# Kernel tuning notes

Hardware: AMD Instinct MI355X
Metric: run time of the kernel (lower is better)

Reference implementation:

```python
import jax, jax.numpy as jnp
import numpy as np

SCORE_THRESH = 0.05
NMS_THRESH = 0.5
K = 1000            # max NMS candidates (fixed for jit; padded/masked)
IMG_W, IMG_H = 1333, 800


def setup_inputs() -> dict:
    key = jax.random.key(0)
    k1, k2, k3 = jax.random.split(key, 3)
    N, C = 200000, 81
    class_logits = jax.random.normal(k1, (N, C), dtype=jnp.float32) * 2.0
    # well-formed xyxy boxes inside the image
    cxcy = jax.random.uniform(k2, (N, 2), dtype=jnp.float32) * jnp.array([IMG_W, IMG_H], jnp.float32)
    wh = jax.random.uniform(k3, (N, 2), dtype=jnp.float32) * 200.0 + 1.0
    boxes = jnp.concatenate([cxcy - wh * 0.5, cxcy + wh * 0.5], axis=-1)
    return {"class_logits": class_logits, "boxes": boxes}


def _pairwise_iou(b):
    # b: [K, 4] xyxy -> [K, K]
    area = (b[:, 2] - b[:, 0]) * (b[:, 3] - b[:, 1])
    lt = jnp.maximum(b[:, None, :2], b[None, :, :2])
    rb = jnp.minimum(b[:, None, 2:], b[None, :, 2:])
    wh = jnp.clip(rb - lt, 0.0)
    inter = wh[..., 0] * wh[..., 1]
    return inter / (area[:, None] + area[None, :] - inter + 1e-9)


def reference(class_logits, boxes):
    N, C = class_logits.shape
    prob = jax.nn.softmax(class_logits, axis=-1)            # [N, C]
    # clip_to_image (TO_REMOVE=1 convention: clamp to size-1)
    bx = jnp.stack([
        jnp.clip(boxes[:, 0], 0.0, IMG_W - 1),
        jnp.clip(boxes[:, 1], 0.0, IMG_H - 1),
        jnp.clip(boxes[:, 2], 0.0, IMG_W - 1),
        jnp.clip(boxes[:, 3], 0.0, IMG_H - 1),
    ], axis=-1)                                             # [N, 4]
    flat = prob.reshape(-1)                                 # [N*C], class = idx % C
    idx = jnp.arange(N * C)
    valid = (flat > SCORE_THRESH) & (idx % C != 0)          # fg + score threshold
    masked = jnp.where(valid, flat, -jnp.inf)
    top_scores, top_idx = jax.lax.top_k(masked, K)          # sorted descending
    prop_idx = top_idx // C
    cls = top_idx % C
    bk = bx[prop_idx]                                       # [K, 4]
    valid_k = jnp.isfinite(top_scores)
    scores_k = jnp.where(valid_k, top_scores, 0.0)
    # class-aware greedy NMS over the (sorted) top-K candidates
    conflict = (_pairwise_iou(bk) > NMS_THRESH) & (cls[:, None] == cls[None, :])
    rng = jnp.arange(K)

    def body(i, keep):
        sup = jnp.any(keep & conflict[:, i] & (rng < i))
        return keep.at[i].set(keep[i] & ~sup)

    keep = jax.lax.fori_loop(0, K, body, valid_k)
    out = jnp.concatenate([bk, scores_k[:, None]], axis=-1) * keep[:, None].astype(bk.dtype)
    return out  # [K, 5]: (x1, y1, x2, y2, score), zeroed where suppressed/invalid
```

## Files before the change

### kernel.cpp

```cpp
#include <hip/hip_runtime.h>
#include <stdint.h>
#include <math.h>

#define N_CLS    81
#define TOPK     1000
#define LISTCAP  (1u << 21)
#define CAP2     16384
#define SCORE_TH 0.05f
#define IMG_W    1333.0f
#define IMG_H    800.0f
#define GH_REP   8

#define GH_BASE  1905

#define OFF_CNT    0
#define OFF_CNT2   8
#define OFF_GH     64
#define OFF_RH     4608
#define OFF_SORTED 8704
#define MEMSET_BYTES 16704
#define OFF_SEL    16768
#define OFF_SEL2   16793984
#define OFF_BOX    16925056
#define OFF_SCORE  16941056
#define OFF_CLS    16945056
#define OFF_MASK   16949056

typedef unsigned long long u64;

__global__ __launch_bounds__(256) void k_pass1(
        const float* __restrict__ logits, int nrows,
        u64* __restrict__ sel, unsigned* __restrict__ cnt,
        unsigned* __restrict__ ghist) {
    __shared__ unsigned lh[128];
    __shared__ u64 cbuf[2048];
    __shared__ unsigned lcnt, gbase;
    int tid = threadIdx.x, wv = tid >> 6, ln = tid & 63;
    for (int i = tid; i < 128; i += 256) lh[i] = 0;
    if (tid == 0) lcnt = 0;
    __syncthreads();

    int stride = gridDim.x * 16;
    for (int base = blockIdx.x * 16 + wv * 4; base < nrows; base += stride) {
        int nr = nrows - base; if (nr > 4) nr = 4;
        float v0[4], v1[4], m[4], e0[4], e1[4], s[4];
        #pragma unroll
        for (int k = 0; k < 4; k++) {
            bool ok = (k < nr);
            const float* rp = logits + (size_t)(ok ? base + k : base) * N_CLS;
            v0[k] = ok ? rp[ln] : 0.0f;
            v1[k] = (ok && ln < N_CLS - 64) ? rp[64 + ln] : -INFINITY;
        }
        #pragma unroll
        for (int k = 0; k < 4; k++) m[k] = fmaxf(v0[k], v1[k]);
        #pragma unroll
        for (int off = 32; off > 0; off >>= 1)
            #pragma unroll
            for (int k = 0; k < 4; k++) m[k] = fmaxf(m[k], __shfl_xor(m[k], off));
        #pragma unroll
        for (int k = 0; k < 4; k++) {
            e0[k] = expf(v0[k] - m[k]);
            e1[k] = (ln < N_CLS - 64) ? expf(v1[k] - m[k]) : 0.0f;
            s[k] = e0[k] + e1[k];
        }
        #pragma unroll
        for (int off = 32; off > 0; off >>= 1)
            #pragma unroll
            for (int k = 0; k < 4; k++) s[k] += __shfl_xor(s[k], off);

        #pragma unroll
        for (int k = 0; k < 4; k++) {
            if (k >= nr) break;
            float p0 = e0[k] / s[k];
            float p1 = e1[k] / s[k];
            bool c0 = (k < nr) && (ln != 0) && (p0 > SCORE_TH);
            bool c1 = (k < nr) && (ln < N_CLS - 64) && (p1 > SCORE_TH);
            unsigned fb0 = __float_as_uint(p0), fb1 = __float_as_uint(p1);
            if (c0) atomicAdd(&lh[(fb0 >> 19) - GH_BASE], 1u);
            if (c1) atomicAdd(&lh[(fb1 >> 19) - GH_BASE], 1u);
            u64 b0 = __ballot(c0), b1 = __ballot(c1);
            int n0 = __popcll(b0), n1 = __popcll(b1);
            if (n0 + n1 == 0) continue;
            unsigned wb = 0;
            if (ln == 0) wb = atomicAdd(&lcnt, (unsigned)(n0 + n1));
            wb = __shfl(wb, 0);
            u64 lt = (1ull << ln) - 1ull;
            unsigned flat = (unsigned)(base + k) * N_CLS + (unsigned)ln;
            if (c0) {
                unsigned pos = wb + (unsigned)__popcll(b0 & lt);
                u64 key = ((u64)fb0 << 32) | (u64)(0xFFFFFFu - flat);
                if (pos < 2048) cbuf[pos] = key;
                else { unsigned gp = atomicAdd(cnt, 1u); if (gp < LISTCAP) sel[gp] = key; }
            }
            if (c1) {
                unsigned pos = wb + (unsigned)n0 + (unsigned)__popcll(b1 & lt);
                u64 key = ((u64)fb1 << 32) | (u64)(0xFFFFFFu - (flat + 64u));
                if (pos < 2048) cbuf[pos] = key;
                else { unsigned gp = atomicAdd(cnt, 1u); if (gp < LISTCAP) sel[gp] = key; }
            }
        }
    }
    __syncthreads();
    unsigned* gh = ghist + (blockIdx.x & (GH_REP - 1)) * 128;
    for (int i = tid; i < 128; i += 256) {
        unsigned v = lh[i];
        if (v) atomicAdd(&gh[i], v);
    }
    unsigned total = lcnt; if (total > 2048u) total = 2048u;
    if (tid == 0) gbase = atomicAdd(cnt, total);
    __syncthreads();
    unsigned gb = gbase;
    for (unsigned i = tid; i < total; i += 256) {
        unsigned gp = gb + i;
        if (gp < LISTCAP) sel[gp] = cbuf[i];
    }
}

__device__ inline int scan_coarse(const unsigned* __restrict__ ghist, unsigned* c_above) {
    unsigned cum = 0;
    for (int i = 127; i >= 0; --i) {
        unsigned c = 0;
        #pragma unroll
        for (int r = 0; r < GH_REP; r++) c += ghist[r * 128 + i];
        if (cum + c >= TOPK) { *c_above = cum; return i; }
        cum += c;
    }
    *c_above = cum;
    return -1;
}

__global__ __launch_bounds__(256) void k_refine(
        const u64* __restrict__ sel, const unsigned* __restrict__ cnt,
        const unsigned* __restrict__ ghist, unsigned* __restrict__ rhist) {
    __shared__ unsigned lh[1024];
    __shared__ int sB;
    int tid = threadIdx.x;
    for (int i = tid; i < 1024; i += 256) lh[i] = 0;
    if (tid == 0) { unsigned ca; sB = scan_coarse(ghist, &ca); }
    __syncthreads();
    int B = sB;
    if (B < 0) return;
    unsigned Bbits = (unsigned)(B + GH_BASE);
    unsigned M = *cnt; if (M > LISTCAP) M = LISTCAP;
    unsigned stride = gridDim.x * blockDim.x;
    for (unsigned i = blockIdx.x * blockDim.x + tid; i < M; i += stride) {
        unsigned bits = (unsigned)(sel[i] >> 32);
        if ((bits >> 19) == Bbits) atomicAdd(&lh[(bits >> 9) & 1023u], 1u);
    }
    __syncthreads();
    for (int i = tid; i < 1024; i += 256) {
        unsigned v = lh[i];
        if (v) atomicAdd(&rhist[i], v);
    }
}

__global__ __launch_bounds__(256) void k_select(
        const u64* __restrict__ sel, const unsigned* __restrict__ cnt,
        const unsigned* __restrict__ ghist, const unsigned* __restrict__ rhist,
        u64* __restrict__ sel2, unsigned* __restrict__ cnt2) {
    __shared__ unsigned s4[256];
    __shared__ unsigned tbs;
    int tid = threadIdx.x, ln = tid & 63;
    unsigned ps = 0;
    #pragma unroll
    for (int k = 0; k < 4; k++) ps += rhist[tid * 4 + k];
    s4[tid] = ps;
    __syncthreads();
    if (tid == 0) {
        unsigned c_above;
        int B = scan_coarse(ghist, &c_above);
        unsigned tb = 0;
        if (B >= 0) {
            unsigned cab = c_above;
            int g = -1;
            for (int i = 255; i >= 0; --i) {
                if (cab + s4[i] >= TOPK) { g = i; break; }
                cab += s4[i];
            }
            int sb = 0;
            if (g >= 0) {
                for (int i = g * 4 + 3; i >= g * 4; --i) {
                    unsigned c = rhist[i];
                    if (cab + c >= TOPK) { sb = i; break; }
                    cab += c;
                }
            }
            tb = ((unsigned)(B + GH_BASE) << 19) | ((unsigned)sb << 9);
        }
        tbs = tb;
    }
    __syncthreads();
    unsigned tb = tbs;
    unsigned M = *cnt; if (M > LISTCAP) M = LISTCAP;
    unsigned stride = gridDim.x * blockDim.x;
    for (unsigned ibase = blockIdx.x * blockDim.x; ibase < M; ibase += stride) {
        unsigned i = ibase + tid;
        bool act = (i < M);
        u64 key = act ? sel[i] : 0ull;
        bool c = act && ((unsigned)(key >> 32) >= tb);
        u64 b = __ballot(c);
        int n = __popcll(b);
        if (n == 0) continue;
        unsigned wb = 0;
        if (ln == 0) wb = atomicAdd(cnt2, (unsigned)n);
        wb = __shfl(wb, 0);
        if (c) {
            unsigned pos = wb + (unsigned)__popcll(b & ((1ull << ln) - 1ull));
            if (pos < CAP2) sel2[pos] = key;
        }
    }
}

__global__ __launch_bounds__(256) void k_rank(
        const u64* __restrict__ sel2, const unsigned* __restrict__ cnt2,
        u64* __restrict__ sorted) {
    __shared__ u64 ch[2048];
    unsigned S = *cnt2; if (S > CAP2) S = CAP2;
    if (blockIdx.x * 256u >= S) return;
    unsigned t = blockIdx.x * 256u + threadIdx.x;
    u64 my = (t < S) ? sel2[t] : 0ull;
    int r = 0;
    for (unsigned c0 = 0; c0 < S; c0 += 2048) {
        unsigned n = S - c0; if (n > 2048) n = 2048;
        __syncthreads();
        for (unsigned i = threadIdx.x; i < n; i += 256) ch[i] = sel2[c0 + i];
        __syncthreads();
        if (t < S)
            for (unsigned j = 0; j < n; j++) r += (ch[j] > my) ? 1 : 0;
    }
    if (t < S && r < TOPK) sorted[r] = my;
}

__global__ __launch_bounds__(256) void k_decode(
        const u64* __restrict__ sorted, const float* __restrict__ boxes,
        float* __restrict__ boxK, float* __restrict__ scoreK, int* __restrict__ clsK) {
    int t = blockIdx.x * blockDim.x + threadIdx.x;
    if (t >= TOPK) return;
    u64 key = sorted[t];
    if (key != 0ull) {
        float sc = __uint_as_float((unsigned)(key >> 32));
        unsigned fi = 0xFFFFFFu - (unsigned)(key & 0xFFFFFFFFull);
        unsigned prop = fi / N_CLS;
        int cls = (int)(fi - prop * N_CLS);
        const float* b = boxes + (size_t)prop * 4;
        boxK[t * 4 + 0] = fminf(fmaxf(b[0], 0.0f), IMG_W - 1.0f);
        boxK[t * 4 + 1] = fminf(fmaxf(b[1], 0.0f), IMG_H - 1.0f);
        boxK[t * 4 + 2] = fminf(fmaxf(b[2], 0.0f), IMG_W - 1.0f);
        boxK[t * 4 + 3] = fminf(fmaxf(b[3], 0.0f), IMG_H - 1.0f);
        scoreK[t] = sc;
        clsK[t] = cls;
    } else {
        boxK[t * 4 + 0] = 0.0f; boxK[t * 4 + 1] = 0.0f;
        boxK[t * 4 + 2] = 0.0f; boxK[t * 4 + 3] = 0.0f;
        scoreK[t] = 0.0f;
        clsK[t] = -1;
    }
}

__global__ __launch_bounds__(256) void k_conflict(
        const float* __restrict__ boxK, const int* __restrict__ clsK,
        u64* __restrict__ mask) {
    int t = blockIdx.x * blockDim.x + threadIdx.x;
    if (t >= TOPK * 16) return;
    int i = t >> 4, w = t & 15;
    float x1 = boxK[i * 4 + 0], y1 = boxK[i * 4 + 1];
    float x2 = boxK[i * 4 + 2], y2 = boxK[i * 4 + 3];
    int ci = clsK[i];
    float ai = (x2 - x1) * (y2 - y1);
    u64 m = 0;
    int jbase = w << 6;
    for (int jj = 0; jj < 64; jj++) {
        int j = jbase + jj;
        if (j >= TOPK) break;
        float u1 = boxK[j * 4 + 0], w1 = boxK[j * 4 + 1];
        float u2 = boxK[j * 4 + 2], w2 = boxK[j * 4 + 3];
        float aj = (u2 - u1) * (w2 - w1);
        float ww = fmaxf(fminf(x2, u2) - fmaxf(x1, u1), 0.0f);
        float hh = fmaxf(fminf(y2, w2) - fmaxf(y1, w1), 0.0f);
        float inter = ww * hh;
        float iou = inter / (ai + aj - inter + 1e-9f);
        if (iou > 0.5f && ci == clsK[j]) m |= (1ull << jj);
    }
    mask[(size_t)i * 16 + w] = m;
}

__global__ __launch_bounds__(1024) void k_nms_out(
        const u64* __restrict__ mask, const float* __restrict__ boxK,
        const float* __restrict__ scoreK, float* __restrict__ out) {
    __shared__ u64 words[16];
    __shared__ int changed;
    int tid = threadIdx.x, wv = tid >> 6, ln = tid & 63;
    bool valid = (tid < TOPK) && (scoreK[tid] > 0.0f);
    u64 row[16];
    #pragma unroll
    for (int w = 0; w < 16; w++)
        row[w] = (tid < TOPK) ? mask[(size_t)tid * 16 + w] : 0ull;
    u64 lowmask = (1ull << ln) - 1ull;
    bool keep = valid;
    for (int it = 0; it < 1024; ++it) {
        u64 b = __ballot(keep);
        if (ln == 0) words[wv] = b;
        if (tid == 0) changed = 0;
        __syncthreads();
        u64 sup = 0;
        for (int w = 0; w <= wv; w++) {
            u64 kw = words[w];
            if (w == wv) kw &= lowmask;
            sup |= row[w] & kw;
        }
        bool nk = valid && (sup == 0ull);
        if (nk != keep) changed = 1;
        keep = nk;
        __syncthreads();
        if (!changed) break;
    }
    if (tid < TOPK) {
        float x1 = boxK[tid * 4 + 0], y1 = boxK[tid * 4 + 1];
        float x2 = boxK[tid * 4 + 2], y2 = boxK[tid * 4 + 3];
        float sc = scoreK[tid];
        out[tid * 5 + 0] = keep ? x1 : 0.0f;
        out[tid * 5 + 1] = keep ? y1 : 0.0f;
        out[tid * 5 + 2] = keep ? x2 : 0.0f;
        out[tid * 5 + 3] = keep ? y2 : 0.0f;
        out[tid * 5 + 4] = keep ? sc : 0.0f;
    }
}

extern "C" void kernel_launch(void* const* d_in, const int* in_sizes, int n_in,
                              void* d_out, int out_size, void* d_ws, size_t ws_size,
                              hipStream_t stream) {
    const float* logits = (const float*)d_in[0];
    const float* boxes  = (const float*)d_in[1];
    float* out = (float*)d_out;
    int nrows = in_sizes[0] / N_CLS;

    char* w = (char*)d_ws;
    unsigned* cnt    = (unsigned*)(w + OFF_CNT);
    unsigned* cnt2   = (unsigned*)(w + OFF_CNT2);
    unsigned* ghist  = (unsigned*)(w + OFF_GH);
    unsigned* rhist  = (unsigned*)(w + OFF_RH);
    u64* sorted      = (u64*)(w + OFF_SORTED);
    u64* sel         = (u64*)(w + OFF_SEL);
    u64* sel2        = (u64*)(w + OFF_SEL2);
    float* boxK      = (float*)(w + OFF_BOX);
    float* scoreK    = (float*)(w + OFF_SCORE);
    int* clsK        = (int*)(w + OFF_CLS);
    u64* mask        = (u64*)(w + OFF_MASK);

    hipMemsetAsync(w, 0, MEMSET_BYTES, stream);

    k_pass1<<<1024, 256, 0, stream>>>(logits, nrows, sel, cnt, ghist);
    k_refine<<<256, 256, 0, stream>>>(sel, cnt, ghist, rhist);
    k_select<<<256, 256, 0, stream>>>(sel, cnt, ghist, rhist, sel2, cnt2);
    k_rank<<<CAP2 / 256, 256, 0, stream>>>(sel2, cnt2, sorted);
    k_decode<<<(TOPK + 255) / 256, 256, 0, stream>>>(sorted, boxes, boxK, scoreK, clsK);
    k_conflict<<<(TOPK * 16 + 255) / 256, 256, 0, stream>>>(boxK, clsK, mask);
    k_nms_out<<<1, 1024, 0, stream>>>(mask, boxK, scoreK, out);
}
```

Baseline: 213.6 us.

## Fuse tail stages into one cooperative kernel with grid syncs

Replaces the six post-pass kernels (refine, select, rank, decode, conflict, NMS) with one cooperative kernel of 256 blocks of 1024 threads, separated by grid.sync barriers, and replaces serial histogram scans with parallel suffix scans. It also doubles the pass-1 grid, halves the shared compaction buffer and doubles histogram replication to reduce atomic contention. The aim is to remove launch gaps and serial single-thread scans between small stages. In exchange it adds grid-wide barrier costs and depends on 256 blocks of 1024 threads being co-resident.

```diff
diff --git a/kernel.cpp b/kernel.cpp
--- a/kernel.cpp
+++ b/kernel.cpp
@@ -1,6 +1,9 @@
 #include <hip/hip_runtime.h>
+#include <hip/hip_cooperative_groups.h>
 #include <stdint.h>
 #include <math.h>
+
+namespace cg = cooperative_groups;
 
 #define N_CLS    81
 #define TOPK     1000
@@ -9,22 +12,22 @@
 #define SCORE_TH 0.05f
 #define IMG_W    1333.0f
 #define IMG_H    800.0f
-#define GH_REP   8
+#define GH_REP   16
 
 #define GH_BASE  1905
 
 #define OFF_CNT    0
 #define OFF_CNT2   8
 #define OFF_GH     64
-#define OFF_RH     4608
-#define OFF_SORTED 8704
-#define MEMSET_BYTES 16704
-#define OFF_SEL    16768
-#define OFF_SEL2   16793984
-#define OFF_BOX    16925056
-#define OFF_SCORE  16941056
-#define OFF_CLS    16945056
-#define OFF_MASK   16949056
+#define OFF_RH     8256
+#define OFF_SORTED 12352
+#define MEMSET_BYTES 20352
+#define OFF_SEL    20480
+#define OFF_SEL2   16797696
+#define OFF_BOX    16928768
+#define OFF_SCORE  16944768
+#define OFF_CLS    16948768
+#define OFF_MASK   16952832
 
 typedef unsigned long long u64;
 
@@ -33,7 +36,7 @@
         u64* __restrict__ sel, unsigned* __restrict__ cnt,
         unsigned* __restrict__ ghist) {
     __shared__ unsigned lh[128];
-    __shared__ u64 cbuf[2048];
+    __shared__ u64 cbuf[1024];
     __shared__ unsigned lcnt, gbase;
     int tid = threadIdx.x, wv = tid >> 6, ln = tid & 63;
     for (int i = tid; i < 128; i += 256) lh[i] = 0;
@@ -89,13 +92,13 @@
             if (c0) {
                 unsigned pos = wb + (unsigned)__popcll(b0 & lt);
                 u64 key = ((u64)fb0 << 32) | (u64)(0xFFFFFFu - flat);
-                if (pos < 2048) cbuf[pos] = key;
+                if (pos < 1024) cbuf[pos] = key;
                 else { unsigned gp = atomicAdd(cnt, 1u); if (gp < LISTCAP) sel[gp] = key; }
             }
             if (c1) {
                 unsigned pos = wb + (unsigned)n0 + (unsigned)__popcll(b1 & lt);
                 u64 key = ((u64)fb1 << 32) | (u64)(0xFFFFFFu - (flat + 64u));
-                if (pos < 2048) cbuf[pos] = key;
+                if (pos < 1024) cbuf[pos] = key;
                 else { unsigned gp = atomicAdd(cnt, 1u); if (gp < LISTCAP) sel[gp] = key; }
             }
         }
@@ -106,7 +109,7 @@
         unsigned v = lh[i];
         if (v) atomicAdd(&gh[i], v);
     }
-    unsigned total = lcnt; if (total > 2048u) total = 2048u;
+    unsigned total = lcnt; if (total > 1024u) total = 1024u;
     if (tid == 0) gbase = atomicAdd(cnt, total);
     __syncthreads();
     unsigned gb = gbase;
@@ -116,180 +119,171 @@
     }
 }
 
-__device__ inline int scan_coarse(const unsigned* __restrict__ ghist, unsigned* c_above) {
-    unsigned cum = 0;
-    for (int i = 127; i >= 0; --i) {
+__global__ __launch_bounds__(1024, 4) void k_tail(
+        const float* __restrict__ boxes,
+        const u64* __restrict__ sel, const unsigned* __restrict__ cnt,
+        const unsigned* __restrict__ ghist, unsigned* __restrict__ rhist,
+        u64* __restrict__ sel2, unsigned* __restrict__ cnt2,
+        u64* __restrict__ sorted,
+        float* __restrict__ boxK, float* __restrict__ scoreK, int* __restrict__ clsK,
+        u64* __restrict__ mask, float* __restrict__ out) {
+    cg::grid_group grid = cg::this_grid();
+    __shared__ u64 ch[2048];
+    __shared__ u64 words[16];
+    __shared__ int sB, sChg;
+    unsigned* cA = (unsigned*)ch;
+    int tid = threadIdx.x, bid = blockIdx.x;
+    int ln = tid & 63, wvi = tid >> 6;
+    unsigned gtid = bid * 1024u + tid;
+    unsigned gstride = gridDim.x * 1024u;
+
+    unsigned M = *cnt; if (M > LISTCAP) M = LISTCAP;
+
+    if (tid < 128) {
         unsigned c = 0;
         #pragma unroll
-        for (int r = 0; r < GH_REP; r++) c += ghist[r * 128 + i];
-        if (cum + c >= TOPK) { *c_above = cum; return i; }
-        cum += c;
-    }
-    *c_above = cum;
-    return -1;
-}
-
-__global__ __launch_bounds__(256) void k_refine(
-        const u64* __restrict__ sel, const unsigned* __restrict__ cnt,
-        const unsigned* __restrict__ ghist, unsigned* __restrict__ rhist) {
-    __shared__ unsigned lh[1024];
-    __shared__ int sB;
-    int tid = threadIdx.x;
-    for (int i = tid; i < 1024; i += 256) lh[i] = 0;
-    if (tid == 0) { unsigned ca; sB = scan_coarse(ghist, &ca); }
+        for (int r = 0; r < GH_REP; r++) c += ghist[r * 128 + tid];
+        cA[tid] = c;
+    }
     __syncthreads();
-    int B = sB;
-    if (B < 0) return;
-    unsigned Bbits = (unsigned)(B + GH_BASE);
-    unsigned M = *cnt; if (M > LISTCAP) M = LISTCAP;
-    unsigned stride = gridDim.x * blockDim.x;
-    for (unsigned i = blockIdx.x * blockDim.x + tid; i < M; i += stride) {
-        unsigned bits = (unsigned)(sel[i] >> 32);
-        if ((bits >> 19) == Bbits) atomicAdd(&lh[(bits >> 9) & 1023u], 1u);
-    }
-    __syncthreads();
-    for (int i = tid; i < 1024; i += 256) {
-        unsigned v = lh[i];
-        if (v) atomicAdd(&rhist[i], v);
-    }
-}
-
-__global__ __launch_bounds__(256) void k_select(
-        const u64* __restrict__ sel, const unsigned* __restrict__ cnt,
-        const unsigned* __restrict__ ghist, const unsigned* __restrict__ rhist,
-        u64* __restrict__ sel2, unsigned* __restrict__ cnt2) {
-    __shared__ unsigned s4[256];
-    __shared__ unsigned tbs;
-    int tid = threadIdx.x, ln = tid & 63;
-    unsigned ps = 0;
-    #pragma unroll
-    for (int k = 0; k < 4; k++) ps += rhist[tid * 4 + k];
-    s4[tid] = ps;
-    __syncthreads();
-    if (tid == 0) {
-        unsigned c_above;
-        int B = scan_coarse(ghist, &c_above);
+    {
+        unsigned* s0 = cA; unsigned* s1 = cA + 128;
+        for (int off = 1; off < 128; off <<= 1) {
+            if (tid < 128) s1[tid] = s0[tid] + ((tid + off < 128) ? s0[tid + off] : 0u);
+            __syncthreads();
+            unsigned* t = s0; s0 = s1; s1 = t;
+        }
+        if (tid == 0) sB = -1;
+        __syncthreads();
+        if (tid < 128 && s0[tid] >= TOPK) atomicMax(&sB, tid);
+        __syncthreads();
+        int B = sB;
+        unsigned c_above = (B >= 0 && B < 127) ? s0[B + 1] : 0u;
+        __syncthreads();
+
+        if (B >= 0) {
+            cA[tid] = 0;
+            __syncthreads();
+            unsigned Bb = (unsigned)(B + GH_BASE);
+            for (unsigned i = gtid; i < M; i += gstride) {
+                unsigned bits = (unsigned)(sel[i] >> 32);
+                if ((bits >> 19) == Bb) atomicAdd(&cA[(bits >> 9) & 1023u], 1u);
+            }
+            __syncthreads();
+            unsigned v = cA[tid];
+            if (v) atomicAdd(&rhist[tid], v);
+        }
+        __threadfence();
+        grid.sync();
+
+        unsigned* a = cA; unsigned* b = cA + 1024;
+        a[tid] = rhist[tid];
+        __syncthreads();
+        unsigned* src = a; unsigned* dst = b;
+        for (int off = 1; off < 1024; off <<= 1) {
+            dst[tid] = src[tid] + ((tid + off < 1024) ? src[tid + off] : 0u);
+            __syncthreads();
+            unsigned* t = src; src = dst; dst = t;
+        }
+        if (tid == 0) sB = -1;
+        __syncthreads();
+        if (B >= 0 && (c_above + src[tid] >= TOPK)) atomicMax(&sB, tid);
+        __syncthreads();
         unsigned tb = 0;
         if (B >= 0) {
-            unsigned cab = c_above;
-            int g = -1;
-            for (int i = 255; i >= 0; --i) {
-                if (cab + s4[i] >= TOPK) { g = i; break; }
-                cab += s4[i];
-            }
-            int sb = 0;
-            if (g >= 0) {
-                for (int i = g * 4 + 3; i >= g * 4; --i) {
-                    unsigned c = rhist[i];
-                    if (cab + c >= TOPK) { sb = i; break; }
-                    cab += c;
+            int sb = sB; if (sb < 0) sb = 0;
+            tb = ((unsigned)(B + GH_BASE) << 19) | ((unsigned)sb << 9);
+        }
+        __syncthreads();
+
+        for (unsigned ib = bid * 1024u; ib < M; ib += gstride) {
+            unsigned i = ib + tid;
+            bool act = (i < M);
+            u64 key = act ? sel[i] : 0ull;
+            bool c = act && ((unsigned)(key >> 32) >= tb);
+            u64 bal = __ballot(c);
+            int n = __popcll(bal);
+            if (n) {
+                unsigned wb = 0;
+                if (ln == 0) wb = atomicAdd(cnt2, (unsigned)n);
+                wb = __shfl(wb, 0);
+                if (c) {
+                    unsigned pos = wb + (unsigned)__popcll(bal & ((1ull << ln) - 1ull));
+                    if (pos < CAP2) sel2[pos] = key;
                 }
             }
-            tb = ((unsigned)(B + GH_BASE) << 19) | ((unsigned)sb << 9);
-        }
-        tbs = tb;
-    }
-    __syncthreads();
-    unsigned tb = tbs;
-    unsigned M = *cnt; if (M > LISTCAP) M = LISTCAP;
-    unsigned stride = gridDim.x * blockDim.x;
-    for (unsigned ibase = blockIdx.x * blockDim.x; ibase < M; ibase += stride) {
-        unsigned i = ibase + tid;
-        bool act = (i < M);
-        u64 key = act ? sel[i] : 0ull;
-        bool c = act && ((unsigned)(key >> 32) >= tb);
-        u64 b = __ballot(c);
-        int n = __popcll(b);
-        if (n == 0) continue;
-        unsigned wb = 0;
-        if (ln == 0) wb = atomicAdd(cnt2, (unsigned)n);
-        wb = __shfl(wb, 0);
-        if (c) {
-            unsigned pos = wb + (unsigned)__popcll(b & ((1ull << ln) - 1ull));
-            if (pos < CAP2) sel2[pos] = key;
-        }
-    }
-}
-
-__global__ __launch_bounds__(256) void k_rank(
-        const u64* __restrict__ sel2, const unsigned* __restrict__ cnt2,
-        u64* __restrict__ sorted) {
-    __shared__ u64 ch[2048];
+        }
+    }
+    __threadfence();
+    grid.sync();
+
     unsigned S = *cnt2; if (S > CAP2) S = CAP2;
-    if (blockIdx.x * 256u >= S) return;
-    unsigned t = blockIdx.x * 256u + threadIdx.x;
-    u64 my = (t < S) ? sel2[t] : 0ull;
-    int r = 0;
-    for (unsigned c0 = 0; c0 < S; c0 += 2048) {
-        unsigned n = S - c0; if (n > 2048) n = 2048;
-        __syncthreads();
-        for (unsigned i = threadIdx.x; i < n; i += 256) ch[i] = sel2[c0 + i];
-        __syncthreads();
-        if (t < S)
-            for (unsigned j = 0; j < n; j++) r += (ch[j] > my) ? 1 : 0;
-    }
-    if (t < S && r < TOPK) sorted[r] = my;
-}
-
-__global__ __launch_bounds__(256) void k_decode(
-        const u64* __restrict__ sorted, const float* __restrict__ boxes,
-        float* __restrict__ boxK, float* __restrict__ scoreK, int* __restrict__ clsK) {
-    int t = blockIdx.x * blockDim.x + threadIdx.x;
-    if (t >= TOPK) return;
-    u64 key = sorted[t];
-    if (key != 0ull) {
-        float sc = __uint_as_float((unsigned)(key >> 32));
-        unsigned fi = 0xFFFFFFu - (unsigned)(key & 0xFFFFFFFFull);
-        unsigned prop = fi / N_CLS;
-        int cls = (int)(fi - prop * N_CLS);
-        const float* b = boxes + (size_t)prop * 4;
-        boxK[t * 4 + 0] = fminf(fmaxf(b[0], 0.0f), IMG_W - 1.0f);
-        boxK[t * 4 + 1] = fminf(fmaxf(b[1], 0.0f), IMG_H - 1.0f);
-        boxK[t * 4 + 2] = fminf(fmaxf(b[2], 0.0f), IMG_W - 1.0f);
-        boxK[t * 4 + 3] = fminf(fmaxf(b[3], 0.0f), IMG_H - 1.0f);
-        scoreK[t] = sc;
-        clsK[t] = cls;
-    } else {
-        boxK[t * 4 + 0] = 0.0f; boxK[t * 4 + 1] = 0.0f;
-        boxK[t * 4 + 2] = 0.0f; boxK[t * 4 + 3] = 0.0f;
-        scoreK[t] = 0.0f;
-        clsK[t] = -1;
-    }
-}
-
-__global__ __launch_bounds__(256) void k_conflict(
-        const float* __restrict__ boxK, const int* __restrict__ clsK,
-        u64* __restrict__ mask) {
-    int t = blockIdx.x * blockDim.x + threadIdx.x;
-    if (t >= TOPK * 16) return;
-    int i = t >> 4, w = t & 15;
-    float x1 = boxK[i * 4 + 0], y1 = boxK[i * 4 + 1];
-    float x2 = boxK[i * 4 + 2], y2 = boxK[i * 4 + 3];
-    int ci = clsK[i];
-    float ai = (x2 - x1) * (y2 - y1);
-    u64 m = 0;
-    int jbase = w << 6;
-    for (int jj = 0; jj < 64; jj++) {
-        int j = jbase + jj;
-        if (j >= TOPK) break;
-        float u1 = boxK[j * 4 + 0], w1 = boxK[j * 4 + 1];
-        float u2 = boxK[j * 4 + 2], w2 = boxK[j * 4 + 3];
-        float aj = (u2 - u1) * (w2 - w1);
-        float ww = fmaxf(fminf(x2, u2) - fmaxf(x1, u1), 0.0f);
-        float hh = fmaxf(fminf(y2, w2) - fmaxf(y1, w1), 0.0f);
-        float inter = ww * hh;
-        float iou = inter / (ai + aj - inter + 1e-9f);
-        if (iou > 0.5f && ci == clsK[j]) m |= (1ull << jj);
-    }
-    mask[(size_t)i * 16 + w] = m;
-}
-
-__global__ __launch_bounds__(1024) void k_nms_out(
-        const u64* __restrict__ mask, const float* __restrict__ boxK,
-        const float* __restrict__ scoreK, float* __restrict__ out) {
-    __shared__ u64 words[16];
-    __shared__ int changed;
-    int tid = threadIdx.x, wv = tid >> 6, ln = tid & 63;
+    if (bid * 1024u < S) {
+        u64 my = (gtid < S) ? sel2[gtid] : 0ull;
+        unsigned r = 0;
+        for (unsigned c0 = 0; c0 < S; c0 += 2048) {
+            unsigned n = S - c0; if (n > 2048u) n = 2048u;
+            __syncthreads();
+            for (unsigned i = tid; i < n; i += 1024) ch[i] = sel2[c0 + i];
+            __syncthreads();
+            if (gtid < S)
+                for (unsigned j = 0; j < n; j++) r += (ch[j] > my) ? 1u : 0u;
+        }
+        if (gtid < S && r < TOPK) sorted[r] = my;
+    }
+    __threadfence();
+    grid.sync();
+
+    if (gtid < TOPK) {
+        u64 key = sorted[gtid];
+        if (key != 0ull) {
+            float sc = __uint_as_float((unsigned)(key >> 32));
+            unsigned fi = 0xFFFFFFu - (unsigned)(key & 0xFFFFFFFFull);
+            unsigned prop = fi / N_CLS;
+            int cls = (int)(fi - prop * N_CLS);
+            const float* bp = boxes + (size_t)prop * 4;
+            boxK[gtid * 4 + 0] = fminf(fmaxf(bp[0], 0.0f), IMG_W - 1.0f);
+            boxK[gtid * 4 + 1] = fminf(fmaxf(bp[1], 0.0f), IMG_H - 1.0f);
+            boxK[gtid * 4 + 2] = fminf(fmaxf(bp[2], 0.0f), IMG_W - 1.0f);
+            boxK[gtid * 4 + 3] = fminf(fmaxf(bp[3], 0.0f), IMG_H - 1.0f);
+            scoreK[gtid] = sc;
+            clsK[gtid] = cls;
+        } else {
+            boxK[gtid * 4 + 0] = 0.0f; boxK[gtid * 4 + 1] = 0.0f;
+            boxK[gtid * 4 + 2] = 0.0f; boxK[gtid * 4 + 3] = 0.0f;
+            scoreK[gtid] = 0.0f;
+            clsK[gtid] = -1;
+        }
+    }
+    __threadfence();
+    grid.sync();
+
+    if (gtid < TOPK * 16u) {
+        int i = (int)(gtid >> 4), w = (int)(gtid & 15u);
+        float x1 = boxK[i * 4 + 0], y1 = boxK[i * 4 + 1];
+        float x2 = boxK[i * 4 + 2], y2 = boxK[i * 4 + 3];
+        int ci = clsK[i];
+        float ai = (x2 - x1) * (y2 - y1);
+        u64 m = 0;
+        int jbase = w << 6;
+        for (int jj = 0; jj < 64; jj++) {
+            int j = jbase + jj;
+            if (j >= TOPK) break;
+            float u1 = boxK[j * 4 + 0], w1 = boxK[j * 4 + 1];
+            float u2 = boxK[j * 4 + 2], w2 = boxK[j * 4 + 3];
+            float aj = (u2 - u1) * (w2 - w1);
+            float ww = fmaxf(fminf(x2, u2) - fmaxf(x1, u1), 0.0f);
+            float hh = fmaxf(fminf(y2, w2) - fmaxf(y1, w1), 0.0f);
+            float inter = ww * hh;
+            float iou = inter / (ai + aj - inter + 1e-9f);
+            if (iou > 0.5f && ci == clsK[j]) m |= (1ull << jj);
+        }
+        mask[(size_t)i * 16 + w] = m;
+    }
+    __threadfence();
+    grid.sync();
+
+    if (bid != 0) return;
     bool valid = (tid < TOPK) && (scoreK[tid] > 0.0f);
     u64 row[16];
     #pragma unroll
@@ -299,20 +293,20 @@
     bool keep = valid;
     for (int it = 0; it < 1024; ++it) {
         u64 b = __ballot(keep);
-        if (ln == 0) words[wv] = b;
-        if (tid == 0) changed = 0;
+        if (ln == 0) words[wvi] = b;
+        if (tid == 0) sChg = 0;
         __syncthreads();
         u64 sup = 0;
-        for (int w = 0; w <= wv; w++) {
+        for (int w = 0; w <= wvi; w++) {
             u64 kw = words[w];
-            if (w == wv) kw &= lowmask;
+            if (w == wvi) kw &= lowmask;
             sup |= row[w] & kw;
         }
         bool nk = valid && (sup == 0ull);
-        if (nk != keep) changed = 1;
+        if (nk != keep) sChg = 1;
         keep = nk;
         __syncthreads();
-        if (!changed) break;
+        if (!sChg) break;
     }
     if (tid < TOPK) {
         float x1 = boxK[tid * 4 + 0], y1 = boxK[tid * 4 + 1];
@@ -349,11 +343,14 @@
 
     hipMemsetAsync(w, 0, MEMSET_BYTES, stream);
 
-    k_pass1<<<1024, 256, 0, stream>>>(logits, nrows, sel, cnt, ghist);
-    k_refine<<<256, 256, 0, stream>>>(sel, cnt, ghist, rhist);
-    k_select<<<256, 256, 0, stream>>>(sel, cnt, ghist, rhist, sel2, cnt2);
-    k_rank<<<CAP2 / 256, 256, 0, stream>>>(sel2, cnt2, sorted);
-    k_decode<<<(TOPK + 255) / 256, 256, 0, stream>>>(sorted, boxes, boxK, scoreK, clsK);
-    k_conflict<<<(TOPK * 16 + 255) / 256, 256, 0, stream>>>(boxK, clsK, mask);
-    k_nms_out<<<1, 1024, 0, stream>>>(mask, boxK, scoreK, out);
+    k_pass1<<<2048, 256, 0, stream>>>(logits, nrows, sel, cnt, ghist);
+
+    void* args[] = {
+        (void*)&boxes, (void*)&sel, (void*)&cnt, (void*)&ghist, (void*)&rhist,
+        (void*)&sel2, (void*)&cnt2, (void*)&sorted,
+        (void*)&boxK, (void*)&scoreK, (void*)&clsK,
+        (void*)&mask, (void*)&out
+    };
+    hipLaunchCooperativeKernel(reinterpret_cast<void*>(k_tail),
+                               dim3(256), dim3(1024), args, 0, stream);
 }
```

Result: slower. 624.8 us (+192.6%).

## Fuse refine/select and decode/conflict stages, defer fine threshold into rank kernel

Applied to the files above, without the earlier changes.

Merges the refine-histogram and select passes into one sweep over the candidate list. Selection now uses only the coarse bucket threshold, so the larger candidate list goes into a bigger sel2 buffer. The fine threshold is computed inside the rank kernel, which drops inactive candidates before counting. Decode is folded into the conflict kernel, which re-decodes boxes from the sorted keys and global memory. Together these cut two launches and one full pass over sel, at the cost of a larger rank workload (more blocks, more O(S^2) compares) and redundant box gathers in the conflict kernel; the pass1 grid and histogram replication are also doubled.

```diff
diff --git a/kernel.cpp b/kernel.cpp
--- a/kernel.cpp
+++ b/kernel.cpp
@@ -5,26 +5,26 @@
 #define N_CLS    81
 #define TOPK     1000
 #define LISTCAP  (1u << 21)
-#define CAP2     16384
+#define CAP2     65536
 #define SCORE_TH 0.05f
 #define IMG_W    1333.0f
 #define IMG_H    800.0f
-#define GH_REP   8
+#define GH_REP   16
 
 #define GH_BASE  1905
 
 #define OFF_CNT    0
 #define OFF_CNT2   8
 #define OFF_GH     64
-#define OFF_RH     4608
-#define OFF_SORTED 8704
-#define MEMSET_BYTES 16704
-#define OFF_SEL    16768
-#define OFF_SEL2   16793984
-#define OFF_BOX    16925056
-#define OFF_SCORE  16941056
-#define OFF_CLS    16945056
-#define OFF_MASK   16949056
+#define OFF_RH     8256
+#define OFF_SORTED 12352
+#define MEMSET_BYTES 20352
+#define OFF_SEL    20480
+#define OFF_SEL2   16797696
+#define OFF_BOX    17321984
+#define OFF_SCORE  17337984
+#define OFF_CLS    17341984
+#define OFF_MASK   17345984
 
 typedef unsigned long long u64;
 
@@ -116,36 +116,56 @@
     }
 }
 
-__device__ inline int scan_coarse(const unsigned* __restrict__ ghist, unsigned* c_above) {
-    unsigned cum = 0;
-    for (int i = 127; i >= 0; --i) {
+__global__ __launch_bounds__(256) void k_select(
+        const u64* __restrict__ sel, const unsigned* __restrict__ cnt,
+        const unsigned* __restrict__ ghist, unsigned* __restrict__ rhist,
+        u64* __restrict__ sel2, unsigned* __restrict__ cnt2) {
+    __shared__ unsigned lh[1024];
+    __shared__ unsigned sc0[128], sc1[128];
+    __shared__ int sB;
+    int tid = threadIdx.x, ln = tid & 63;
+    for (int i = tid; i < 1024; i += 256) lh[i] = 0;
+    if (tid < 128) {
         unsigned c = 0;
         #pragma unroll
-        for (int r = 0; r < GH_REP; r++) c += ghist[r * 128 + i];
-        if (cum + c >= TOPK) { *c_above = cum; return i; }
-        cum += c;
-    }
-    *c_above = cum;
-    return -1;
-}
-
-__global__ __launch_bounds__(256) void k_refine(
-        const u64* __restrict__ sel, const unsigned* __restrict__ cnt,
-        const unsigned* __restrict__ ghist, unsigned* __restrict__ rhist) {
-    __shared__ unsigned lh[1024];
-    __shared__ int sB;
-    int tid = threadIdx.x;
-    for (int i = tid; i < 1024; i += 256) lh[i] = 0;
-    if (tid == 0) { unsigned ca; sB = scan_coarse(ghist, &ca); }
+        for (int r = 0; r < GH_REP; r++) c += ghist[r * 128 + tid];
+        sc0[tid] = c;
+    }
+    if (tid == 0) sB = -1;
+    __syncthreads();
+    unsigned *s0 = sc0, *s1 = sc1;
+    for (int off = 1; off < 128; off <<= 1) {
+        if (tid < 128) s1[tid] = s0[tid] + ((tid + off < 128) ? s0[tid + off] : 0u);
+        __syncthreads();
+        unsigned* t = s0; s0 = s1; s1 = t;
+    }
+    if (tid < 128 && s0[tid] >= TOPK) atomicMax(&sB, tid);
     __syncthreads();
     int B = sB;
-    if (B < 0) return;
-    unsigned Bbits = (unsigned)(B + GH_BASE);
+    unsigned tb = (B >= 0) ? ((unsigned)(B + GH_BASE) << 19) : 0u;
+    unsigned Bb = (unsigned)(B + GH_BASE);
+
     unsigned M = *cnt; if (M > LISTCAP) M = LISTCAP;
-    unsigned stride = gridDim.x * blockDim.x;
-    for (unsigned i = blockIdx.x * blockDim.x + tid; i < M; i += stride) {
-        unsigned bits = (unsigned)(sel[i] >> 32);
-        if ((bits >> 19) == Bbits) atomicAdd(&lh[(bits >> 9) & 1023u], 1u);
+    unsigned gstride = gridDim.x * 256u;
+    for (unsigned ib = blockIdx.x * 256u; ib < M; ib += gstride) {
+        unsigned i = ib + tid;
+        bool act = (i < M);
+        u64 key = act ? sel[i] : 0ull;
+        unsigned bits = (unsigned)(key >> 32);
+        bool c = act && (bits >= tb);
+        if (c && B >= 0 && (bits >> 19) == Bb)
+            atomicAdd(&lh[(bits >> 9) & 1023u], 1u);
+        u64 bal = __ballot(c);
+        int n = __popcll(bal);
+        if (n) {
+            unsigned wb = 0;
+            if (ln == 0) wb = atomicAdd(cnt2, (unsigned)n);
+            wb = __shfl(wb, 0);
+            if (c) {
+                unsigned pos = wb + (unsigned)__popcll(bal & ((1ull << ln) - 1ull));
+                if (pos < CAP2) sel2[pos] = key;
+            }
+        }
     }
     __syncthreads();
     for (int i = tid; i < 1024; i += 256) {
@@ -154,132 +174,134 @@
     }
 }
 
-__global__ __launch_bounds__(256) void k_select(
-        const u64* __restrict__ sel, const unsigned* __restrict__ cnt,
+__global__ __launch_bounds__(256) void k_rank(
+        const u64* __restrict__ sel2, const unsigned* __restrict__ cnt2,
         const unsigned* __restrict__ ghist, const unsigned* __restrict__ rhist,
-        u64* __restrict__ sel2, unsigned* __restrict__ cnt2) {
-    __shared__ unsigned s4[256];
+        u64* __restrict__ sorted) {
+    __shared__ u64 ch[2048];
+    __shared__ unsigned sa[256], sb_[256];
+    __shared__ int sB, sG;
     __shared__ unsigned tbs;
-    int tid = threadIdx.x, ln = tid & 63;
+    int tid = threadIdx.x;
+
+    if (tid < 128) {
+        unsigned c = 0;
+        #pragma unroll
+        for (int r = 0; r < GH_REP; r++) c += ghist[r * 128 + tid];
+        sa[tid] = c;
+    }
+    if (tid == 0) { sB = -1; sG = -1; }
+    __syncthreads();
+    unsigned *s0 = sa, *s1 = sb_;
+    for (int off = 1; off < 128; off <<= 1) {
+        if (tid < 128) s1[tid] = s0[tid] + ((tid + off < 128) ? s0[tid + off] : 0u);
+        __syncthreads();
+        unsigned* t = s0; s0 = s1; s1 = t;
+    }
+    if (tid < 128 && s0[tid] >= TOPK) atomicMax(&sB, tid);
+    __syncthreads();
+    int B = sB;
+    unsigned c_above = (B >= 0 && B < 127) ? s0[B + 1] : 0u;
+    __syncthreads();
+
     unsigned ps = 0;
     #pragma unroll
     for (int k = 0; k < 4; k++) ps += rhist[tid * 4 + k];
-    s4[tid] = ps;
+    sa[tid] = ps;
+    __syncthreads();
+    s0 = sa; s1 = sb_;
+    for (int off = 1; off < 256; off <<= 1) {
+        s1[tid] = s0[tid] + ((tid + off < 256) ? s0[tid + off] : 0u);
+        __syncthreads();
+        unsigned* t = s0; s0 = s1; s1 = t;
+    }
+    if (B >= 0 && c_above + s0[tid] >= TOPK) atomicMax(&sG, tid);
     __syncthreads();
     if (tid == 0) {
-        unsigned c_above;
-        int B = scan_coarse(ghist, &c_above);
         unsigned tb = 0;
         if (B >= 0) {
-            unsigned cab = c_above;
-            int g = -1;
-            for (int i = 255; i >= 0; --i) {
-                if (cab + s4[i] >= TOPK) { g = i; break; }
-                cab += s4[i];
-            }
-            int sb = 0;
+            int g = sG;
+            int sbin = 0;
             if (g >= 0) {
+                unsigned cab = c_above + ((g < 255) ? s0[g + 1] : 0u);
                 for (int i = g * 4 + 3; i >= g * 4; --i) {
                     unsigned c = rhist[i];
-                    if (cab + c >= TOPK) { sb = i; break; }
+                    if (cab + c >= TOPK) { sbin = i; break; }
                     cab += c;
                 }
             }
-            tb = ((unsigned)(B + GH_BASE) << 19) | ((unsigned)sb << 9);
+            tb = ((unsigned)(B + GH_BASE) << 19) | ((unsigned)sbin << 9);
         }
         tbs = tb;
     }
     __syncthreads();
     unsigned tb = tbs;
-    unsigned M = *cnt; if (M > LISTCAP) M = LISTCAP;
-    unsigned stride = gridDim.x * blockDim.x;
-    for (unsigned ibase = blockIdx.x * blockDim.x; ibase < M; ibase += stride) {
-        unsigned i = ibase + tid;
-        bool act = (i < M);
-        u64 key = act ? sel[i] : 0ull;
-        bool c = act && ((unsigned)(key >> 32) >= tb);
-        u64 b = __ballot(c);
-        int n = __popcll(b);
-        if (n == 0) continue;
-        unsigned wb = 0;
-        if (ln == 0) wb = atomicAdd(cnt2, (unsigned)n);
-        wb = __shfl(wb, 0);
-        if (c) {
-            unsigned pos = wb + (unsigned)__popcll(b & ((1ull << ln) - 1ull));
-            if (pos < CAP2) sel2[pos] = key;
-        }
-    }
-}
-
-__global__ __launch_bounds__(256) void k_rank(
-        const u64* __restrict__ sel2, const unsigned* __restrict__ cnt2,
-        u64* __restrict__ sorted) {
-    __shared__ u64 ch[2048];
+
     unsigned S = *cnt2; if (S > CAP2) S = CAP2;
-    if (blockIdx.x * 256u >= S) return;
-    unsigned t = blockIdx.x * 256u + threadIdx.x;
+    unsigned t = blockIdx.x * 256u + tid;
     u64 my = (t < S) ? sel2[t] : 0ull;
-    int r = 0;
+    bool active = (t < S) && ((unsigned)(my >> 32) >= tb);
+    unsigned r = 0;
     for (unsigned c0 = 0; c0 < S; c0 += 2048) {
-        unsigned n = S - c0; if (n > 2048) n = 2048;
-        __syncthreads();
-        for (unsigned i = threadIdx.x; i < n; i += 256) ch[i] = sel2[c0 + i];
-        __syncthreads();
-        if (t < S)
-            for (unsigned j = 0; j < n; j++) r += (ch[j] > my) ? 1 : 0;
-    }
-    if (t < S && r < TOPK) sorted[r] = my;
-}
-
-__global__ __launch_bounds__(256) void k_decode(
+        unsigned n = S - c0; if (n > 2048u) n = 2048u;
+        __syncthreads();
+        for (unsigned i = tid; i < n; i += 256) ch[i] = sel2[c0 + i];
+        __syncthreads();
+        if (active)
+            for (unsigned j = 0; j < n; j++) r += (ch[j] > my) ? 1u : 0u;
+    }
+    if (active && r < TOPK) sorted[r] = my;
+}
+
+__global__ __launch_bounds__(256) void k_conflict(
         const u64* __restrict__ sorted, const float* __restrict__ boxes,
-        float* __restrict__ boxK, float* __restrict__ scoreK, int* __restrict__ clsK) {
-    int t = blockIdx.x * blockDim.x + threadIdx.x;
-    if (t >= TOPK) return;
-    u64 key = sorted[t];
+        float* __restrict__ boxK, float* __restrict__ scoreK, int* __restrict__ clsK,
+        u64* __restrict__ mask) {
+    int t = blockIdx.x * 256 + threadIdx.x;
+    if (t >= TOPK * 16) return;
+    int i = t >> 4, w = t & 15;
+    u64 key = sorted[i];
+    float x1 = 0.0f, y1 = 0.0f, x2 = 0.0f, y2 = 0.0f, sc = 0.0f;
+    int ci = -1;
     if (key != 0ull) {
-        float sc = __uint_as_float((unsigned)(key >> 32));
+        sc = __uint_as_float((unsigned)(key >> 32));
         unsigned fi = 0xFFFFFFu - (unsigned)(key & 0xFFFFFFFFull);
         unsigned prop = fi / N_CLS;
-        int cls = (int)(fi - prop * N_CLS);
-        const float* b = boxes + (size_t)prop * 4;
-        boxK[t * 4 + 0] = fminf(fmaxf(b[0], 0.0f), IMG_W - 1.0f);
-        boxK[t * 4 + 1] = fminf(fmaxf(b[1], 0.0f), IMG_H - 1.0f);
-        boxK[t * 4 + 2] = fminf(fmaxf(b[2], 0.0f), IMG_W - 1.0f);
-        boxK[t * 4 + 3] = fminf(fmaxf(b[3], 0.0f), IMG_H - 1.0f);
-        scoreK[t] = sc;
-        clsK[t] = cls;
-    } else {
-        boxK[t * 4 + 0] = 0.0f; boxK[t * 4 + 1] = 0.0f;
-        boxK[t * 4 + 2] = 0.0f; boxK[t * 4 + 3] = 0.0f;
-        scoreK[t] = 0.0f;
-        clsK[t] = -1;
-    }
-}
-
-__global__ __launch_bounds__(256) void k_conflict(
-        const float* __restrict__ boxK, const int* __restrict__ clsK,
-        u64* __restrict__ mask) {
-    int t = blockIdx.x * blockDim.x + threadIdx.x;
-    if (t >= TOPK * 16) return;
-    int i = t >> 4, w = t & 15;
-    float x1 = boxK[i * 4 + 0], y1 = boxK[i * 4 + 1];
-    float x2 = boxK[i * 4 + 2], y2 = boxK[i * 4 + 3];
-    int ci = clsK[i];
+        ci = (int)(fi - prop * N_CLS);
+        const float* bp = boxes + (size_t)prop * 4;
+        x1 = fminf(fmaxf(bp[0], 0.0f), IMG_W - 1.0f);
+        y1 = fminf(fmaxf(bp[1], 0.0f), IMG_H - 1.0f);
+        x2 = fminf(fmaxf(bp[2], 0.0f), IMG_W - 1.0f);
+        y2 = fminf(fmaxf(bp[3], 0.0f), IMG_H - 1.0f);
+    }
+    if (w == 0) {
+        boxK[i * 4 + 0] = x1; boxK[i * 4 + 1] = y1;
+        boxK[i * 4 + 2] = x2; boxK[i * 4 + 3] = y2;
+        scoreK[i] = sc;
+        clsK[i] = ci;
+    }
     float ai = (x2 - x1) * (y2 - y1);
     u64 m = 0;
     int jbase = w << 6;
     for (int jj = 0; jj < 64; jj++) {
         int j = jbase + jj;
         if (j >= TOPK) break;
-        float u1 = boxK[j * 4 + 0], w1 = boxK[j * 4 + 1];
-        float u2 = boxK[j * 4 + 2], w2 = boxK[j * 4 + 3];
+        u64 kj = sorted[j];
+        if (kj == 0ull) continue;
+        unsigned fj = 0xFFFFFFu - (unsigned)(kj & 0xFFFFFFFFull);
+        unsigned pj = fj / N_CLS;
+        int cj = (int)(fj - pj * N_CLS);
+        const float* bq = boxes + (size_t)pj * 4;
+        float u1 = fminf(fmaxf(bq[0], 0.0f), IMG_W - 1.0f);
+        float w1 = fminf(fmaxf(bq[1], 0.0f), IMG_H - 1.0f);
+        float u2 = fminf(fmaxf(bq[2], 0.0f), IMG_W - 1.0f);
+        float w2 = fminf(fmaxf(bq[3], 0.0f), IMG_H - 1.0f);
         float aj = (u2 - u1) * (w2 - w1);
         float ww = fmaxf(fminf(x2, u2) - fmaxf(x1, u1), 0.0f);
         float hh = fmaxf(fminf(y2, w2) - fmaxf(y1, w1), 0.0f);
         float inter = ww * hh;
         float iou = inter / (ai + aj - inter + 1e-9f);
-        if (iou > 0.5f && ci == clsK[j]) m |= (1ull << jj);
+        if (iou > 0.5f && ci == cj) m |= (1ull << jj);
     }
     mask[(size_t)i * 16 + w] = m;
 }
@@ -349,11 +371,9 @@
 
     hipMemsetAsync(w, 0, MEMSET_BYTES, stream);
 
-    k_pass1<<<1024, 256, 0, stream>>>(logits, nrows, sel, cnt, ghist);
-    k_refine<<<256, 256, 0, stream>>>(sel, cnt, ghist, rhist);
+    k_pass1<<<2048, 256, 0, stream>>>(logits, nrows, sel, cnt, ghist);
     k_select<<<256, 256, 0, stream>>>(sel, cnt, ghist, rhist, sel2, cnt2);
-    k_rank<<<CAP2 / 256, 256, 0, stream>>>(sel2, cnt2, sorted);
-    k_decode<<<(TOPK + 255) / 256, 256, 0, stream>>>(sorted, boxes, boxK, scoreK, clsK);
-    k_conflict<<<(TOPK * 16 + 255) / 256, 256, 0, stream>>>(boxK, clsK, mask);
+    k_rank<<<CAP2 / 256, 256, 0, stream>>>(sel2, cnt2, ghist, rhist, sorted);
+    k_conflict<<<(TOPK * 16 + 255) / 256, 256, 0, stream>>>(sorted, boxes, boxK, scoreK, clsK, mask);
     k_nms_out<<<1, 1024, 0, stream>>>(mask, boxK, scoreK, out);
 }
```

Measured after the change: 236.2 us. +10.6%, slower.
